# Optimization experiments

Measured on AMD Instinct MI355X. Metric: run time of the kernel, lower is better.

## Reference

```python
import jax, jax.numpy as jnp
import numpy as np

N = 262144      # total nodes
E = 1048576     # total edges
G = 8192        # num graphs (= batch[-1]+1)
H = 128         # hidden
L = 4           # layers
VA = 64         # atom feature vocab
VB = 8          # bond feature vocab
FA = 9          # atom feature columns
FB = 3          # bond feature columns
BN_EPS = 1e-5


def _bn(x, g, b, m, v):
    # BatchNorm1d in eval mode: running stats
    return (x - m) * jax.lax.rsqrt(v + BN_EPS) * g + b


def setup_inputs() -> dict:
    key = jax.random.key(0)
    ks = jax.random.split(key, 40)
    rn = lambda k, s, sc=0.05: jax.random.normal(k, s, dtype=jnp.float32) * sc
    x = jax.random.randint(ks[0], (N, FA), 0, VA)
    edge_index = jax.random.randint(ks[1], (2, E), 0, N)
    edge_attr = jax.random.randint(ks[2], (E, FB), 0, VB)
    batch = jnp.sort(jax.random.randint(ks[3], (N,), 0, G))
    batch = batch.at[0].set(0).at[-1].set(G - 1)
    params = dict(
        atom_emb=rn(ks[4], (FA, VA, H)),
        vn_emb=rn(ks[5], (H,)),
        bond_emb=rn(ks[6], (L, FB, VB, H)),
        conv_eps=rn(ks[7], (L,)),
        conv_W1=rn(ks[8], (L, H, 2 * H)), conv_b1=rn(ks[9], (L, 2 * H)),
        conv_bn_g=1.0 + rn(ks[10], (L, 2 * H)), conv_bn_b=rn(ks[11], (L, 2 * H)),
        conv_bn_m=rn(ks[12], (L, 2 * H), 0.1),
        conv_bn_v=0.5 + jax.random.uniform(ks[13], (L, 2 * H)) * 0.5,
        conv_W2=rn(ks[14], (L, 2 * H, H)), conv_b2=rn(ks[15], (L, H)),
        vn1_W=rn(ks[16], (L, 2 * H, 2 * H)), vn1_b=rn(ks[17], (L, 2 * H)),
        vn1_g=1.0 + rn(ks[18], (L, 2 * H)), vn1_be=rn(ks[19], (L, 2 * H)),
        vn1_m=rn(ks[20], (L, 2 * H), 0.1),
        vn1_v=0.5 + jax.random.uniform(ks[21], (L, 2 * H)) * 0.5,
        vn2_W=rn(ks[22], (L, 2 * H, H)), vn2_b=rn(ks[23], (L, H)),
        vn2_g=1.0 + rn(ks[24], (L, H)), vn2_be=rn(ks[25], (L, H)),
        vn2_m=rn(ks[26], (L, H), 0.1),
        vn2_v=0.5 + jax.random.uniform(ks[27], (L, H)) * 0.5,
        pW1=rn(ks[28], (H, H)), pb1=rn(ks[29], (H,)),
        pW2=rn(ks[30], (H, 1)), pb2=rn(ks[31], (1,)),
    )
    return dict(x=x, edge_index=edge_index, edge_attr=edge_attr, batch=batch, **params)


def reference(x, edge_index, edge_attr, batch, atom_emb, vn_emb, bond_emb,
              conv_eps, conv_W1, conv_b1, conv_bn_g, conv_bn_b, conv_bn_m, conv_bn_v,
              conv_W2, conv_b2, vn1_W, vn1_b, vn1_g, vn1_be, vn1_m, vn1_v,
              vn2_W, vn2_b, vn2_g, vn2_be, vn2_m, vn2_v, pW1, pb1, pW2, pb2):
    src, dst = edge_index[0], edge_index[1]
    # AtomEncoder: sum of per-feature embeddings -> [N, H]
    h = atom_emb[jnp.arange(FA)[:, None], x.T].sum(0)
    # virtual node embedding broadcast to all graphs: [G, H]
    vn = jnp.broadcast_to(vn_emb, (G, H))
    for i in range(L):
        h = h + vn[batch]
        # CombConv (GIN-with-edge-features): msg = relu(x_j + bond_emb)
        e = bond_emb[i][jnp.arange(FB)[:, None], edge_attr.T].sum(0)  # [E, H]
        msg = jax.nn.relu(h[src] + e)
        agg = jax.ops.segment_sum(msg, dst, num_segments=N)  # [N, H]
        z = (1.0 + conv_eps[i]) * h + agg
        z = jax.nn.relu(_bn(z @ conv_W1[i] + conv_b1[i],
                            conv_bn_g[i], conv_bn_b[i], conv_bn_m[i], conv_bn_v[i]))
        h = z @ conv_W2[i] + conv_b2[i]
        # virtual node update: gather-concat-MLP, pool, MLP
        t = jnp.concatenate([vn[batch], h], axis=-1)  # [N, 2H]
        t = jax.nn.relu(_bn(t @ vn1_W[i] + vn1_b[i],
                            vn1_g[i], vn1_be[i], vn1_m[i], vn1_v[i]))
        pooled = jax.ops.segment_sum(t, batch, num_segments=G)  # [G, 2H]
        vn = jax.nn.relu(_bn(pooled @ vn2_W[i] + vn2_b[i],
                             vn2_g[i], vn2_be[i], vn2_m[i], vn2_v[i]))
    # JK='L': last virtual-node representation; dropout=0
    out = jax.nn.relu(vn @ pW1 + pb1) @ pW2 + pb2  # [G, 1]
    return jnp.clip(out, 0.0, 50.0)  # eval-mode clamp
```

## Files before the change

### kernel.cpp

```cpp
#include <hip/hip_runtime.h>
#include <hip/hip_fp16.h>

#define NN 262144
#define EE 1048576
#define GG 8192
#define HH 128
#define FBc 3
#define VAc 64
#define VBc 8
#define FAc 9

typedef _Float16 f16;
typedef _Float16 f16x8 __attribute__((ext_vector_type(8)));
typedef float f32x4 __attribute__((ext_vector_type(4)));

__device__ __forceinline__ float h2f(ushort u) {
    __half h; *(ushort*)&h = u; return __half2float(h);
}
__device__ __forceinline__ ushort f2h(float f) {
    __half h = __float2half_rn(f); return *(ushort*)&h;
}
__device__ __forceinline__ int swz(int col, int row) {
    return (((col >> 3) ^ (row & 7)) << 3) | (col & 7);
}

__global__ void k_zero(float* __restrict__ p) {
    size_t i = (size_t)(blockIdx.x * 256 + threadIdx.x) * 4;
    *(float4*)(p + i) = make_float4(0.f, 0.f, 0.f, 0.f);
}

__global__ void k_atom(const int* __restrict__ x, const float* __restrict__ emb,
                       ushort* __restrict__ h16) {
    int t = blockIdx.x * 256 + threadIdx.x;
    int n = t >> 5, c = (t & 31) << 2;
    if (n >= NN) return;
    float4 a = make_float4(0.f, 0.f, 0.f, 0.f);
#pragma unroll
    for (int f = 0; f < FAc; ++f) {
        int v = x[n * FAc + f];
        float4 e = *(const float4*)(emb + ((size_t)(f * VAc + v)) * HH + c);
        a.x += e.x; a.y += e.y; a.z += e.z; a.w += e.w;
    }
    ushort4 o;
    o.x = f2h(a.x * 0.0625f); o.y = f2h(a.y * 0.0625f);
    o.z = f2h(a.z * 0.0625f); o.w = f2h(a.w * 0.0625f);
    *(ushort4*)(h16 + (size_t)n * HH + c) = o;
}

__global__ void k_init_vn(const float* __restrict__ vn_emb, float* __restrict__ vn) {
    int t = blockIdx.x * 256 + threadIdx.x;
    int g = t >> 5, c = (t & 31) << 2;
    *(float4*)(vn + (size_t)g * HH + c) = *(const float4*)(vn_emb + c);
}

__global__ void k_hist(const int* __restrict__ ei, int* __restrict__ deg) {
    int e = blockIdx.x * 256 + threadIdx.x;
    atomicAdd(&deg[ei[EE + e]], 1);
}
__global__ void k_scan1(const int* __restrict__ deg, int* __restrict__ rowptr,
                        int* __restrict__ sums) {
    __shared__ int s[256];
    int base = blockIdx.x * 1024 + threadIdx.x * 4;
    int4 d = *(const int4*)(deg + base);
    int t = d.x + d.y + d.z + d.w;
    s[threadIdx.x] = t;
    __syncthreads();
    for (int off = 1; off < 256; off <<= 1) {
        int v = (threadIdx.x >= off) ? s[threadIdx.x - off] : 0;
        __syncthreads();
        s[threadIdx.x] += v;
        __syncthreads();
    }
    int excl = s[threadIdx.x] - t;
    int4 o; o.x = excl; o.y = excl + d.x; o.z = o.y + d.y; o.w = o.z + d.z;
    *(int4*)(rowptr + base) = o;
    if (threadIdx.x == 255) sums[blockIdx.x] = s[255];
}
__global__ void k_scan2(int* __restrict__ sums) {
    __shared__ int s[256];
    int t = sums[threadIdx.x];
    s[threadIdx.x] = t;
    __syncthreads();
    for (int off = 1; off < 256; off <<= 1) {
        int v = (threadIdx.x >= off) ? s[threadIdx.x - off] : 0;
        __syncthreads();
        s[threadIdx.x] += v;
        __syncthreads();
    }
    sums[threadIdx.x] = s[threadIdx.x] - t;
}
__global__ void k_scan3(int* __restrict__ rowptr, const int* __restrict__ sums,
                        int* __restrict__ fill) {
    int base = blockIdx.x * 1024 + threadIdx.x * 4;
    int add = sums[blockIdx.x];
    int4 r = *(const int4*)(rowptr + base);
    r.x += add; r.y += add; r.z += add; r.w += add;
    *(int4*)(rowptr + base) = r;
    *(int4*)(fill + base) = r;
    if (blockIdx.x == 0 && threadIdx.x == 0) rowptr[NN] = EE;
}
__global__ void k_scatter(const int* __restrict__ ei, const int* __restrict__ ea,
                          int* __restrict__ fill, unsigned* __restrict__ packed) {
    int e = blockIdx.x * 256 + threadIdx.x;
    int dst = ei[EE + e];
    int pos = atomicAdd(&fill[dst], 1);
    unsigned cb = (unsigned)(ea[e * 3 + 0] + ea[e * 3 + 1] * 8 + ea[e * 3 + 2] * 64);
    packed[pos] = (unsigned)ei[e] | (cb << 18);
}

__global__ void k_setup(const float* __restrict__ bemb, float* __restrict__ ctab,
                        const float* __restrict__ b1, const float* __restrict__ g1,
                        const float* __restrict__ be1, const float* __restrict__ m1,
                        const float* __restrict__ v1,
                        const float* __restrict__ g3, const float* __restrict__ be3,
                        const float* __restrict__ m3, const float* __restrict__ v3,
                        float* __restrict__ ZA, float* __restrict__ ZB,
                        float* __restrict__ TA, float* __restrict__ TB,
                        float* __restrict__ S3,
                        const float* __restrict__ W1, ushort* __restrict__ W1t,
                        const float* __restrict__ W2, ushort* __restrict__ W2t,
                        const float* __restrict__ W3, ushort* __restrict__ W3t,
                        const float* __restrict__ vn, ushort* __restrict__ vn16,
                        float* __restrict__ pooled) {
    int t = blockIdx.x * 256 + threadIdx.x;
    if (t < 16384) {
        int cb = t >> 5, c = (t & 31) << 2;
        int a0 = cb & 7, a1 = (cb >> 3) & 7, a2 = cb >> 6;
        float4 b0 = *(const float4*)(bemb + (size_t)(0 * VBc + a0) * HH + c);
        float4 b1v = *(const float4*)(bemb + (size_t)(1 * VBc + a1) * HH + c);
        float4 b2v = *(const float4*)(bemb + (size_t)(2 * VBc + a2) * HH + c);
        *(float4*)(ctab + (size_t)cb * HH + c) =
            make_float4(b0.x + b1v.x + b2v.x, b0.y + b1v.y + b2v.y,
                        b0.z + b1v.z + b2v.z, b0.w + b1v.w + b2v.w);
    } else if (t < 16640) {
        int c = t - 16384;
        float s1 = g1[c] * rsqrtf(v1[c] + 1e-5f);
        ZA[c] = s1;
        ZB[c] = ((b1[c] - m1[c]) * s1 + be1[c]) * 0.0625f;
        float s3 = g3[c] * rsqrtf(v3[c] + 1e-5f);
        TA[c] = 16.f * s3;
        TB[c] = be3[c] - m3[c] * s3;
        S3[c] = s3;
    } else if (t < 278784) {
        int i4 = t - 16640;
        float4 v = *(const float4*)(vn + (size_t)i4 * 4);
        ushort4 o;
        o.x = f2h(v.x * 0.0625f); o.y = f2h(v.y * 0.0625f);
        o.z = f2h(v.z * 0.0625f); o.w = f2h(v.w * 0.0625f);
        *(ushort4*)(vn16 + (size_t)i4 * 4) = o;
    } else if (t < 311552) {
        int o = t - 278784;
        int c = o >> 7, k = o & 127;
        W1t[o] = f2h(W1[(size_t)k * 256 + c]);
    } else if (t < 344320) {
        int o = t - 311552;
        int c = o >> 8, k = o & 255;
        W2t[o] = f2h(W2[(size_t)k * 128 + c]);
    } else if (t < 377088) {
        int o = t - 344320;
        int c = o >> 7, k = o & 127;
        W3t[o] = f2h(W3[(size_t)k * 256 + c]);
    } else {
        int i4 = t - 377088;
        *(float4*)(pooled + (size_t)i4 * 4) = make_float4(0.f, 0.f, 0.f, 0.f);
    }
}

__global__ void k_agg(const ushort* __restrict__ h16, const ushort* __restrict__ vn16,
                      const int* __restrict__ batch,
                      const int* __restrict__ rowptr, const unsigned* __restrict__ packed,
                      const float* __restrict__ ctab, ushort* __restrict__ agg) {
    int n = blockIdx.x * 4 + (threadIdx.x >> 6);
    int lane = threadIdx.x & 63;
    int co = lane * 2;
    int beg = rowptr[n], end = rowptr[n + 1];
    float a0 = 0.f, a1 = 0.f;
    int i = beg;
    for (; i + 1 < end; i += 2) {
        unsigned p0 = packed[i], p1 = packed[i + 1];
        int s0 = p0 & 0x3FFFF, s1 = p1 & 0x3FFFF;
        int c0 = p0 >> 18, c1 = p1 >> 18;
        ushort2 u0 = *(const ushort2*)(h16 + (size_t)s0 * HH + co);
        ushort2 u1 = *(const ushort2*)(h16 + (size_t)s1 * HH + co);
        ushort2 w0 = *(const ushort2*)(vn16 + (size_t)batch[s0] * HH + co);
        ushort2 w1 = *(const ushort2*)(vn16 + (size_t)batch[s1] * HH + co);
        float2 t0 = *(const float2*)(ctab + (size_t)c0 * HH + co);
        float2 t1 = *(const float2*)(ctab + (size_t)c1 * HH + co);
        a0 += fmaxf(16.f * (h2f(u0.x) + h2f(w0.x)) + t0.x, 0.f)
            + fmaxf(16.f * (h2f(u1.x) + h2f(w1.x)) + t1.x, 0.f);
        a1 += fmaxf(16.f * (h2f(u0.y) + h2f(w0.y)) + t0.y, 0.f)
            + fmaxf(16.f * (h2f(u1.y) + h2f(w1.y)) + t1.y, 0.f);
    }
    if (i < end) {
        unsigned p = packed[i];
        int src = p & 0x3FFFF, cb = p >> 18;
        ushort2 u = *(const ushort2*)(h16 + (size_t)src * HH + co);
        ushort2 wv = *(const ushort2*)(vn16 + (size_t)batch[src] * HH + co);
        float2 ct = *(const float2*)(ctab + (size_t)cb * HH + co);
        a0 += fmaxf(16.f * (h2f(u.x) + h2f(wv.x)) + ct.x, 0.f);
        a1 += fmaxf(16.f * (h2f(u.y) + h2f(wv.y)) + ct.y, 0.f);
    }
    ushort2 o; o.x = f2h(a0 * 0.0625f); o.y = f2h(a1 * 0.0625f);
    *(ushort2*)(agg + (size_t)n * HH + co) = o;
}

__global__ void __launch_bounds__(256, 3)
k_conv(ushort* __restrict__ h16, const ushort* __restrict__ agg,
       const ushort* __restrict__ W1t, const ushort* __restrict__ W2t,
       const ushort* __restrict__ W3t,
       const int* __restrict__ batch, const ushort* __restrict__ vn16,
       const float* __restrict__ vnW,
       const float* __restrict__ eps_ptr,
       const float* __restrict__ ZA, const float* __restrict__ ZB,
       const float* __restrict__ b2,
       const float* __restrict__ TA, const float* __restrict__ TB,
       float* __restrict__ pooled) {
    __shared__ ushort zs[64][256];
    __shared__ ushort Wb[64][128];
    ushort(*Wb2)[256] = (ushort(*)[256]) & Wb[0][0];
    const int tid = threadIdx.x;
    const int r0 = blockIdx.x * 64;
    const int w = tid >> 6, l = tid & 63, lr = l & 15, lg = l >> 4, lr7 = lr & 7;
    const float eps1 = 1.f + eps_ptr[0];
    const int myrow = w * 16 + lr;
    const int growA = r0 + myrow;
    const int ggA = batch[growA];
    int rl[4], ggs[4];
#pragma unroll
    for (int reg = 0; reg < 4; ++reg) {
        rl[reg] = w * 16 + lg * 4 + reg;
        ggs[reg] = batch[r0 + rl[reg]];
    }

    f16x8 af[4];
#pragma unroll
    for (int k0 = 0; k0 < 4; ++k0) {
        int ko = k0 * 32 + lg * 8;
        f16x8 hv = *(const f16x8*)(h16 + (size_t)growA * HH + ko);
        f16x8 vv = *(const f16x8*)(vn16 + (size_t)ggA * HH + ko);
        f16x8 ag = *(const f16x8*)(agg + (size_t)growA * HH + ko);
#pragma unroll
        for (int j = 0; j < 8; ++j)
            af[k0][j] = (f16)(eps1 * ((float)hv[j] + (float)vv[j]) + (float)ag[j]);
    }

    for (int qt = 0; qt < 4; ++qt) {
        __syncthreads();
        {
            int c = tid >> 2, q = tid & 3, c7 = c & 7;
            const ushort* s = W1t + (size_t)(qt * 64 + c) * 128 + q * 32;
#pragma unroll
            for (int j4 = 0; j4 < 4; ++j4)
                *(f16x8*)&Wb[c][((q * 4 + j4) ^ c7) << 3] = *(const f16x8*)(s + j4 * 8);
        }
        __syncthreads();
        f32x4 acc[4] = {};
#pragma unroll
        for (int k0 = 0; k0 < 4; ++k0) {
            int sb = ((k0 * 4 + lg) ^ lr7) << 3;
#pragma unroll
            for (int fc = 0; fc < 4; ++fc) {
                f16x8 bf = *(const f16x8*)&Wb[fc * 16 + lr][sb];
                acc[fc] = __builtin_amdgcn_mfma_f32_16x16x32_f16(af[k0], bf, acc[fc], 0, 0, 0);
            }
        }
#pragma unroll
        for (int fc = 0; fc < 4; ++fc) {
            int col = qt * 64 + fc * 16 + lr;
            float za = ZA[col], zb = ZB[col];
#pragma unroll
            for (int reg = 0; reg < 4; ++reg) {
                float zv = fmaxf(acc[fc][reg] * za + zb, 0.f);
                zs[rl[reg]][swz(col, rl[reg])] = f2h(zv);
            }
        }
    }

    f32x4 acc2[8] = {};
    for (int st = 0; st < 4; ++st) {
        __syncthreads();
        {
            int c = tid >> 3, q = tid & 7, c7 = c & 7;
            const ushort* s = W2t + (size_t)(st * 32 + c) * 256 + q * 32;
#pragma unroll
            for (int j4 = 0; j4 < 4; ++j4)
                *(f16x8*)&Wb2[c][((q * 4 + j4) ^ c7) << 3] = *(const f16x8*)(s + j4 * 8);
        }
        __syncthreads();
#pragma unroll
        for (int k0 = 0; k0 < 8; ++k0) {
            int sb = ((k0 * 4 + lg) ^ lr7) << 3;
            f16x8 az = *(const f16x8*)&zs[myrow][sb];
#pragma unroll
            for (int fc = 0; fc < 2; ++fc) {
                f16x8 bf = *(const f16x8*)&Wb2[fc * 16 + lr][sb];
                acc2[st * 2 + fc] =
                    __builtin_amdgcn_mfma_f32_16x16x32_f16(az, bf, acc2[st * 2 + fc], 0, 0, 0);
            }
        }
    }
    __syncthreads();
#pragma unroll
    for (int st = 0; st < 4; ++st) {
#pragma unroll
        for (int fc = 0; fc < 2; ++fc) {
            int col = st * 32 + fc * 16 + lr;
            float bb = b2[col];
#pragma unroll
            for (int reg = 0; reg < 4; ++reg) {
                float hv = acc2[st * 2 + fc][reg] * 16.f + bb;
                zs[rl[reg]][swz(col, rl[reg])] = f2h(hv * 0.0625f);
            }
        }
    }
    {
        int row = tid >> 2, q = tid & 3, r7 = row & 7;
#pragma unroll
        for (int j4 = 0; j4 < 4; ++j4) {
            f16x8 v = *(const f16x8*)&zs[row][((q * 4 + j4) ^ r7) << 3];
            *(f16x8*)(h16 + (size_t)(r0 + row) * HH + q * 32 + j4 * 8) = v;
        }
    }

    for (int pr = 0; pr < 2; ++pr) {
#pragma unroll
        for (int sub = 0; sub < 2; ++sub) {
            int qt = pr * 2 + sub;
            __syncthreads();
            {
                int c = tid >> 2, q = tid & 3, c7 = c & 7;
                const ushort* s = W3t + (size_t)(qt * 64 + c) * 128 + q * 32;
#pragma unroll
                for (int j4 = 0; j4 < 4; ++j4)
                    *(f16x8*)&Wb[c][((q * 4 + j4) ^ c7) << 3] = *(const f16x8*)(s + j4 * 8);
            }
            __syncthreads();
            f32x4 acc3[4] = {};
#pragma unroll
            for (int k0 = 0; k0 < 4; ++k0) {
                int sb = ((k0 * 4 + lg) ^ lr7) << 3;
                f16x8 ah = *(const f16x8*)&zs[myrow][sb];
#pragma unroll
                for (int fc = 0; fc < 4; ++fc) {
                    f16x8 bf = *(const f16x8*)&Wb[fc * 16 + lr][sb];
                    acc3[fc] = __builtin_amdgcn_mfma_f32_16x16x32_f16(ah, bf, acc3[fc], 0, 0, 0);
                }
            }
#pragma unroll
            for (int fc = 0; fc < 4; ++fc) {
                int colg = qt * 64 + fc * 16 + lr;
                int colL = 128 + sub * 64 + fc * 16 + lr;
                float ta = TA[colg], tb = TB[colg];
#pragma unroll
                for (int reg = 0; reg < 4; ++reg) {
                    float tv = fmaxf(acc3[fc][reg] * ta + vnW[(size_t)ggs[reg] * 256 + colg] + tb, 0.f);
                    zs[rl[reg]][swz(colL, rl[reg])] = f2h(tv);
                }
            }
        }
        __syncthreads();
        {
            int c = tid & 127, half = tid >> 7;
            int gcol = pr * 128 + c;
            int colL = 128 + c;
            float s = 0.f;
            int cur = batch[r0 + half * 32];
            for (int r = half * 32; r < half * 32 + 32; ++r) {
                int gg = batch[r0 + r];
                if (gg != cur) {
                    atomicAdd(&pooled[(size_t)cur * 256 + gcol], s);
                    s = 0.f; cur = gg;
                }
                s += h2f(zs[r][swz(colL, r)]);
            }
            atomicAdd(&pooled[(size_t)cur * 256 + gcol], s);
        }
        __syncthreads();
    }
}

enum { E_BIAS = 0, E_BNRELU = 1 };
template <int EMODE>
__global__ void __launch_bounds__(256)
gemm_k(const void* __restrict__ Av, const float* __restrict__ B,
       const float* __restrict__ bias,
       const float* __restrict__ g_, const float* __restrict__ b_,
       const float* __restrict__ m_, const float* __restrict__ v_,
       const float* __restrict__ scp,
       void* __restrict__ outv, int K, int Nc) {
    __shared__ float As[64][33];
    __shared__ float Bs[32][64];
    const int tid = threadIdx.x;
    const int row0 = blockIdx.x * 64;
    const int col0 = blockIdx.y * 64;
    float acc[4][4] = {};
    const int tx = tid & 15, ty = tid >> 4;
    for (int k0 = 0; k0 < K; k0 += 32) {
#pragma unroll
        for (int p = 0; p < 2; ++p) {
            int idx = p * 256 + tid;
            {
                int r = idx >> 3, c = (idx & 7) << 2;
                size_t aoff = (size_t)(row0 + r) * K + k0 + c;
                float4 va = *(const float4*)((const float*)Av + aoff);
                As[r][c + 0] = va.x; As[r][c + 1] = va.y;
                As[r][c + 2] = va.z; As[r][c + 3] = va.w;
            }
            {
                int kr = idx >> 4, cc = (idx & 15) << 2;
                *(float4*)&Bs[kr][cc] =
                    *(const float4*)(B + (size_t)(k0 + kr) * Nc + col0 + cc);
            }
        }
        __syncthreads();
#pragma unroll
        for (int k = 0; k < 32; ++k) {
            float4 bv = *(const float4*)&Bs[k][tx << 2];
            float a0 = As[ty * 4 + 0][k];
            float a1 = As[ty * 4 + 1][k];
            float a2 = As[ty * 4 + 2][k];
            float a3 = As[ty * 4 + 3][k];
            acc[0][0] += a0 * bv.x; acc[0][1] += a0 * bv.y; acc[0][2] += a0 * bv.z; acc[0][3] += a0 * bv.w;
            acc[1][0] += a1 * bv.x; acc[1][1] += a1 * bv.y; acc[1][2] += a1 * bv.z; acc[1][3] += a1 * bv.w;
            acc[2][0] += a2 * bv.x; acc[2][1] += a2 * bv.y; acc[2][2] += a2 * bv.z; acc[2][3] += a2 * bv.w;
            acc[3][0] += a3 * bv.x; acc[3][1] += a3 * bv.y; acc[3][2] += a3 * bv.z; acc[3][3] += a3 * bv.w;
        }
        __syncthreads();
    }
#pragma unroll
    for (int j = 0; j < 4; ++j) {
        int gr = row0 + ty * 4 + j;
        float vals[4];
#pragma unroll
        for (int lx = 0; lx < 4; ++lx) {
            int gc = col0 + (tx << 2) + lx;
            float val = acc[j][lx];
            if (EMODE == E_BIAS) {
                float v = val + bias[gc];
                if (scp) v *= scp[gc];
                vals[lx] = v;
            } else {
                float y = val + bias[gc];
                float s = g_[gc] * rsqrtf(v_[gc] + 1e-5f);
                y = (y - m_[gc]) * s + b_[gc];
                vals[lx] = fmaxf(y, 0.f);
            }
        }
        *(float4*)((float*)outv + (size_t)gr * Nc + col0 + (tx << 2)) =
            make_float4(vals[0], vals[1], vals[2], vals[3]);
    }
}

__global__ void k_final(const float* __restrict__ vn, const float* __restrict__ pW1,
                        const float* __restrict__ pb1, const float* __restrict__ pW2,
                        const float* __restrict__ pb2, float* __restrict__ out) {
    int g = blockIdx.x;
    int j = threadIdx.x;
    __shared__ float vrow[HH];
    __shared__ float red[HH];
    vrow[j] = vn[(size_t)g * HH + j];
    __syncthreads();
    float acc = pb1[j];
    for (int k = 0; k < HH; ++k) acc = fmaf(vrow[k], pW1[k * HH + j], acc);
    red[j] = fmaxf(acc, 0.f) * pW2[j];
    __syncthreads();
    for (int s = 64; s > 0; s >>= 1) {
        if (j < s) red[j] += red[j + s];
        __syncthreads();
    }
    if (j == 0) out[g] = fminf(fmaxf(red[0] + pb2[0], 0.f), 50.f);
}

extern "C" void kernel_launch(void* const* d_in, const int* in_sizes, int n_in,
                              void* d_out, int out_size, void* d_ws, size_t ws_size,
                              hipStream_t stream) {
    const int*   x        = (const int*)  d_in[0];
    const int*   ei       = (const int*)  d_in[1];
    const int*   ea       = (const int*)  d_in[2];
    const int*   batch    = (const int*)  d_in[3];
    const float* atom_emb = (const float*)d_in[4];
    const float* vn_emb   = (const float*)d_in[5];
    const float* bond_emb = (const float*)d_in[6];
    const float* conv_eps = (const float*)d_in[7];
    const float* conv_W1  = (const float*)d_in[8];
    const float* conv_b1  = (const float*)d_in[9];
    const float* cbn_g    = (const float*)d_in[10];
    const float* cbn_b    = (const float*)d_in[11];
    const float* cbn_m    = (const float*)d_in[12];
    const float* cbn_v    = (const float*)d_in[13];
    const float* conv_W2  = (const float*)d_in[14];
    const float* conv_b2  = (const float*)d_in[15];
    const float* vn1_W    = (const float*)d_in[16];
    const float* vn1_b    = (const float*)d_in[17];
    const float* vn1_g    = (const float*)d_in[18];
    const float* vn1_be   = (const float*)d_in[19];
    const float* vn1_m    = (const float*)d_in[20];
    const float* vn1_v    = (const float*)d_in[21];
    const float* vn2_W    = (const float*)d_in[22];
    const float* vn2_b    = (const float*)d_in[23];
    const float* vn2_g    = (const float*)d_in[24];
    const float* vn2_be   = (const float*)d_in[25];
    const float* vn2_m    = (const float*)d_in[26];
    const float* vn2_v    = (const float*)d_in[27];
    const float* pW1      = (const float*)d_in[28];
    const float* pb1      = (const float*)d_in[29];
    const float* pW2      = (const float*)d_in[30];
    const float* pb2      = (const float*)d_in[31];

    char* base = (char*)d_ws;
    ushort*   h16    = (ushort*)base;
    ushort*   agg    = h16 + (size_t)NN * HH;
    unsigned* packed = (unsigned*)(agg + (size_t)NN * HH);
    int*      rowptr = (int*)(packed + EE);
    int*      fill   = rowptr + NN + 4;
    float*    ctab   = (float*)(fill + NN);
    int*      sums   = (int*)(ctab + 512 * HH);
    ushort*   W1t    = (ushort*)(sums + 256);
    ushort*   W2t    = W1t + 256 * 128;
    ushort*   W3t    = W2t + 128 * 256;
    float*    ZA     = (float*)(W3t + 256 * 128);
    float*    ZB     = ZA + 256;
    float*    TA     = ZB + 256;
    float*    TB     = TA + 256;
    float*    S3     = TB + 256;
    float*    vn     = S3 + 256;
    ushort*   vn16   = (ushort*)(vn + (size_t)GG * HH);
    float*    vnW    = (float*)(vn16 + (size_t)GG * HH);
    float*    pooled = vnW + (size_t)GG * 256;
    float*    out    = (float*)d_out;

    k_zero<<<256, 256, 0, stream>>>((float*)fill);
    k_hist<<<EE / 256, 256, 0, stream>>>(ei, fill);
    k_scan1<<<256, 256, 0, stream>>>(fill, rowptr, sums);
    k_scan2<<<1, 256, 0, stream>>>(sums);
    k_scan3<<<256, 256, 0, stream>>>(rowptr, sums, fill);
    k_scatter<<<EE / 256, 256, 0, stream>>>(ei, ea, fill, packed);
    k_atom<<<NN * 32 / 256, 256, 0, stream>>>(x, atom_emb, h16);
    k_init_vn<<<GG * HH / 4 / 256, 256, 0, stream>>>(vn_emb, vn);

    for (int i = 0; i < 4; ++i) {
        k_setup<<<3521, 256, 0, stream>>>(
            bond_emb + (size_t)i * FBc * VBc * HH, ctab,
            conv_b1 + i * 256, cbn_g + i * 256, cbn_b + i * 256,
            cbn_m + i * 256, cbn_v + i * 256,
            vn1_g + i * 256, vn1_be + i * 256, vn1_m + i * 256, vn1_v + i * 256,
            ZA, ZB, TA, TB, S3,
            conv_W1 + (size_t)i * HH * 256, W1t,
            conv_W2 + (size_t)i * 256 * HH, W2t,
            vn1_W + (size_t)i * 256 * 256 + 128 * 256, W3t,
            vn, vn16, pooled);

        k_agg<<<NN / 4, 256, 0, stream>>>(h16, vn16, batch, rowptr, packed, ctab, agg);

        {
            dim3 g3(GG / 64, 4);
            gemm_k<E_BIAS><<<g3, 256, 0, stream>>>(
                vn, vn1_W + (size_t)i * 256 * 256, vn1_b + i * 256,
                nullptr, nullptr, nullptr, nullptr, S3, vnW, HH, 256);
        }

        k_conv<<<NN / 64, 256, 0, stream>>>(
            h16, agg, W1t, W2t, W3t, batch, vn16, vnW, conv_eps + i,
            ZA, ZB, conv_b2 + i * HH, TA, TB, pooled);

        {
            dim3 g4(GG / 64, 2);
            gemm_k<E_BNRELU><<<g4, 256, 0, stream>>>(
                pooled, vn2_W + (size_t)i * 256 * HH, vn2_b + i * HH,
                vn2_g + i * HH, vn2_be + i * HH, vn2_m + i * HH, vn2_v + i * HH,
                nullptr, vn, 256, HH);
        }
    }
    k_final<<<GG, 128, 0, stream>>>(vn, pW1, pb1, pW2, pb2, out);
}
```

Baseline: 1.547 ms.

## Fuse edge aggregation into conv kernel with ping-pong node buffers

Removes the separate k_agg kernel and computes the per-node message sum inside k_conv. Each 16-lane group handles four rows, gathering 8 channels per lane with 16-byte loads, and writes the result into shared memory instead of a global agg buffer. The bond-combination table is now stored in fp16 pre-scaled by 1/16, which shrinks gather traffic. h16 is double-buffered so the conv kernel can read neighbours' old features while writing new ones. This saves one launch and the global agg round trip, but the gather phase now runs inside an occupancy-limited GEMM kernel with a block-wide barrier, so latency hiding may suffer.

```diff
diff --git a/kernel.cpp b/kernel.cpp
--- a/kernel.cpp
+++ b/kernel.cpp
@@ -108,7 +108,7 @@
     packed[pos] = (unsigned)ei[e] | (cb << 18);
 }
 
-__global__ void k_setup(const float* __restrict__ bemb, float* __restrict__ ctab,
+__global__ void k_setup(const float* __restrict__ bemb, ushort* __restrict__ ct16,
                         const float* __restrict__ b1, const float* __restrict__ g1,
                         const float* __restrict__ be1, const float* __restrict__ m1,
                         const float* __restrict__ v1,
@@ -129,9 +129,12 @@
         float4 b0 = *(const float4*)(bemb + (size_t)(0 * VBc + a0) * HH + c);
         float4 b1v = *(const float4*)(bemb + (size_t)(1 * VBc + a1) * HH + c);
         float4 b2v = *(const float4*)(bemb + (size_t)(2 * VBc + a2) * HH + c);
-        *(float4*)(ctab + (size_t)cb * HH + c) =
-            make_float4(b0.x + b1v.x + b2v.x, b0.y + b1v.y + b2v.y,
-                        b0.z + b1v.z + b2v.z, b0.w + b1v.w + b2v.w);
+        ushort4 o;
+        o.x = f2h((b0.x + b1v.x + b2v.x) * 0.0625f);
+        o.y = f2h((b0.y + b1v.y + b2v.y) * 0.0625f);
+        o.z = f2h((b0.z + b1v.z + b2v.z) * 0.0625f);
+        o.w = f2h((b0.w + b1v.w + b2v.w) * 0.0625f);
+        *(ushort4*)(ct16 + (size_t)cb * HH + c) = o;
     } else if (t < 16640) {
         int c = t - 16384;
         float s1 = g1[c] * rsqrtf(v1[c] + 1e-5f);
@@ -166,46 +169,10 @@
     }
 }
 
-__global__ void k_agg(const ushort* __restrict__ h16, const ushort* __restrict__ vn16,
-                      const int* __restrict__ batch,
-                      const int* __restrict__ rowptr, const unsigned* __restrict__ packed,
-                      const float* __restrict__ ctab, ushort* __restrict__ agg) {
-    int n = blockIdx.x * 4 + (threadIdx.x >> 6);
-    int lane = threadIdx.x & 63;
-    int co = lane * 2;
-    int beg = rowptr[n], end = rowptr[n + 1];
-    float a0 = 0.f, a1 = 0.f;
-    int i = beg;
-    for (; i + 1 < end; i += 2) {
-        unsigned p0 = packed[i], p1 = packed[i + 1];
-        int s0 = p0 & 0x3FFFF, s1 = p1 & 0x3FFFF;
-        int c0 = p0 >> 18, c1 = p1 >> 18;
-        ushort2 u0 = *(const ushort2*)(h16 + (size_t)s0 * HH + co);
-        ushort2 u1 = *(const ushort2*)(h16 + (size_t)s1 * HH + co);
-        ushort2 w0 = *(const ushort2*)(vn16 + (size_t)batch[s0] * HH + co);
-        ushort2 w1 = *(const ushort2*)(vn16 + (size_t)batch[s1] * HH + co);
-        float2 t0 = *(const float2*)(ctab + (size_t)c0 * HH + co);
-        float2 t1 = *(const float2*)(ctab + (size_t)c1 * HH + co);
-        a0 += fmaxf(16.f * (h2f(u0.x) + h2f(w0.x)) + t0.x, 0.f)
-            + fmaxf(16.f * (h2f(u1.x) + h2f(w1.x)) + t1.x, 0.f);
-        a1 += fmaxf(16.f * (h2f(u0.y) + h2f(w0.y)) + t0.y, 0.f)
-            + fmaxf(16.f * (h2f(u1.y) + h2f(w1.y)) + t1.y, 0.f);
-    }
-    if (i < end) {
-        unsigned p = packed[i];
-        int src = p & 0x3FFFF, cb = p >> 18;
-        ushort2 u = *(const ushort2*)(h16 + (size_t)src * HH + co);
-        ushort2 wv = *(const ushort2*)(vn16 + (size_t)batch[src] * HH + co);
-        float2 ct = *(const float2*)(ctab + (size_t)cb * HH + co);
-        a0 += fmaxf(16.f * (h2f(u.x) + h2f(wv.x)) + ct.x, 0.f);
-        a1 += fmaxf(16.f * (h2f(u.y) + h2f(wv.y)) + ct.y, 0.f);
-    }
-    ushort2 o; o.x = f2h(a0 * 0.0625f); o.y = f2h(a1 * 0.0625f);
-    *(ushort2*)(agg + (size_t)n * HH + co) = o;
-}
-
 __global__ void __launch_bounds__(256, 3)
-k_conv(ushort* __restrict__ h16, const ushort* __restrict__ agg,
+k_conv(const ushort* __restrict__ h16in, ushort* __restrict__ h16out,
+       const int* __restrict__ rowptr, const unsigned* __restrict__ packed,
+       const ushort* __restrict__ ct16,
        const ushort* __restrict__ W1t, const ushort* __restrict__ W2t,
        const ushort* __restrict__ W3t,
        const int* __restrict__ batch, const ushort* __restrict__ vn16,
@@ -232,13 +199,55 @@
         ggs[reg] = batch[r0 + rl[reg]];
     }
 
+    {
+        int grp = tid >> 4, ln = tid & 15;
+        int ch0 = ln * 8;
+        for (int rr = 0; rr < 4; ++rr) {
+            int row = grp * 4 + rr;
+            int beg = rowptr[r0 + row], end = rowptr[r0 + row + 1];
+            float ac[8] = {0.f, 0.f, 0.f, 0.f, 0.f, 0.f, 0.f, 0.f};
+            int e = beg;
+            for (; e + 1 < end; e += 2) {
+                unsigned p0 = packed[e], p1 = packed[e + 1];
+                int s0 = p0 & 0x3FFFF, s1 = p1 & 0x3FFFF;
+                int c0 = p0 >> 18, c1 = p1 >> 18;
+                f16x8 h0 = *(const f16x8*)(h16in + (size_t)s0 * HH + ch0);
+                f16x8 h1 = *(const f16x8*)(h16in + (size_t)s1 * HH + ch0);
+                f16x8 v0 = *(const f16x8*)(vn16 + (size_t)batch[s0] * HH + ch0);
+                f16x8 v1 = *(const f16x8*)(vn16 + (size_t)batch[s1] * HH + ch0);
+                f16x8 t0 = *(const f16x8*)(ct16 + (size_t)c0 * HH + ch0);
+                f16x8 t1 = *(const f16x8*)(ct16 + (size_t)c1 * HH + ch0);
+#pragma unroll
+                for (int j = 0; j < 8; ++j) {
+                    ac[j] += fmaxf((float)h0[j] + (float)v0[j] + (float)t0[j], 0.f)
+                           + fmaxf((float)h1[j] + (float)v1[j] + (float)t1[j], 0.f);
+                }
+            }
+            if (e < end) {
+                unsigned p = packed[e];
+                int src = p & 0x3FFFF, cb = p >> 18;
+                f16x8 hv = *(const f16x8*)(h16in + (size_t)src * HH + ch0);
+                f16x8 vv = *(const f16x8*)(vn16 + (size_t)batch[src] * HH + ch0);
+                f16x8 ct = *(const f16x8*)(ct16 + (size_t)cb * HH + ch0);
+#pragma unroll
+                for (int j = 0; j < 8; ++j)
+                    ac[j] += fmaxf((float)hv[j] + (float)vv[j] + (float)ct[j], 0.f);
+            }
+            f16x8 o;
+#pragma unroll
+            for (int j = 0; j < 8; ++j) o[j] = (f16)ac[j];
+            *(f16x8*)&zs[row][((ch0 >> 3) ^ (row & 7)) << 3] = o;
+        }
+    }
+    __syncthreads();
+
     f16x8 af[4];
 #pragma unroll
     for (int k0 = 0; k0 < 4; ++k0) {
         int ko = k0 * 32 + lg * 8;
-        f16x8 hv = *(const f16x8*)(h16 + (size_t)growA * HH + ko);
+        f16x8 hv = *(const f16x8*)(h16in + (size_t)growA * HH + ko);
         f16x8 vv = *(const f16x8*)(vn16 + (size_t)ggA * HH + ko);
-        f16x8 ag = *(const f16x8*)(agg + (size_t)growA * HH + ko);
+        f16x8 ag = *(const f16x8*)&zs[myrow][((ko >> 3) ^ (myrow & 7)) << 3];
 #pragma unroll
         for (int j = 0; j < 8; ++j)
             af[k0][j] = (f16)(eps1 * ((float)hv[j] + (float)vv[j]) + (float)ag[j]);
@@ -318,7 +327,7 @@
 #pragma unroll
         for (int j4 = 0; j4 < 4; ++j4) {
             f16x8 v = *(const f16x8*)&zs[row][((q * 4 + j4) ^ r7) << 3];
-            *(f16x8*)(h16 + (size_t)(r0 + row) * HH + q * 32 + j4 * 8) = v;
+            *(f16x8*)(h16out + (size_t)(r0 + row) * HH + q * 32 + j4 * 8) = v;
         }
     }
 
@@ -508,13 +517,13 @@
     const float* pb2      = (const float*)d_in[31];
 
     char* base = (char*)d_ws;
-    ushort*   h16    = (ushort*)base;
-    ushort*   agg    = h16 + (size_t)NN * HH;
-    unsigned* packed = (unsigned*)(agg + (size_t)NN * HH);
+    ushort*   h16a   = (ushort*)base;
+    ushort*   h16b   = h16a + (size_t)NN * HH;
+    unsigned* packed = (unsigned*)(h16b + (size_t)NN * HH);
     int*      rowptr = (int*)(packed + EE);
     int*      fill   = rowptr + NN + 4;
-    float*    ctab   = (float*)(fill + NN);
-    int*      sums   = (int*)(ctab + 512 * HH);
+    ushort*   ct16   = (ushort*)(fill + NN);
+    int*      sums   = (int*)(ct16 + 512 * HH);
     ushort*   W1t    = (ushort*)(sums + 256);
     ushort*   W2t    = W1t + 256 * 128;
     ushort*   W3t    = W2t + 128 * 256;
@@ -535,12 +544,15 @@
     k_scan2<<<1, 256, 0, stream>>>(sums);
     k_scan3<<<256, 256, 0, stream>>>(rowptr, sums, fill);
     k_scatter<<<EE / 256, 256, 0, stream>>>(ei, ea, fill, packed);
-    k_atom<<<NN * 32 / 256, 256, 0, stream>>>(x, atom_emb, h16);
+    k_atom<<<NN * 32 / 256, 256, 0, stream>>>(x, atom_emb, h16a);
     k_init_vn<<<GG * HH / 4 / 256, 256, 0, stream>>>(vn_emb, vn);
 
     for (int i = 0; i < 4; ++i) {
+        ushort* hin  = (i & 1) ? h16b : h16a;
+        ushort* hout = (i & 1) ? h16a : h16b;
+
         k_setup<<<3521, 256, 0, stream>>>(
-            bond_emb + (size_t)i * FBc * VBc * HH, ctab,
+            bond_emb + (size_t)i * FBc * VBc * HH, ct16,
             conv_b1 + i * 256, cbn_g + i * 256, cbn_b + i * 256,
             cbn_m + i * 256, cbn_v + i * 256,
             vn1_g + i * 256, vn1_be + i * 256, vn1_m + i * 256, vn1_v + i * 256,
@@ -550,8 +562,6 @@
             vn1_W + (size_t)i * 256 * 256 + 128 * 256, W3t,
             vn, vn16, pooled);
 
-        k_agg<<<NN / 4, 256, 0, stream>>>(h16, vn16, batch, rowptr, packed, ctab, agg);
-
         {
             dim3 g3(GG / 64, 4);
             gemm_k<E_BIAS><<<g3, 256, 0, stream>>>(
@@ -560,7 +570,8 @@
         }
 
         k_conv<<<NN / 64, 256, 0, stream>>>(
-            h16, agg, W1t, W2t, W3t, batch, vn16, vnW, conv_eps + i,
+            hin, hout, rowptr, packed, ct16,
+            W1t, W2t, W3t, batch, vn16, vnW, conv_eps + i,
             ZA, ZB, conv_b2 + i * HH, TA, TB, pooled);
 
         {
```

Measured after the change: 1.543 ms. No clear change (-0.2%).
